# Kernel tuning notes

Measured on AMD Instinct MI355X. Metric: run time of the kernel, lower is better.

## Reference

```python
import jax, jax.numpy as jnp
import numpy as np

B, N, VF, EF, DV, DE, LN = 64, 64, 32, 16, 128, 128, 4
EPS_INNER = 128.0  # BatchNorm1d(MAX_N, internal_d_vert): 2nd positional arg is eps (faithful to source bug)
EPS_BN = 1e-5


def gev_layer(v_in, e_in, evW, evb, eW, eb, vW, vb, relu=True):
    act = jax.nn.relu if relu else (lambda x: x)
    ev = v_in @ evW + evb                                   # [B,N,De]
    # outer_v_sum: ev.unsqueeze(1) + ev.unsqueeze(2) -> [B,N,N,De]
    e_out = act(e_in @ eW + eb + ev[:, None, :, :] + ev[:, :, None, :])
    per_v_e = e_out.sum(axis=1)                             # sum-aggregate over dim 1
    v_out = act(jnp.concatenate([per_v_e, v_in], axis=-1) @ vW + vb)
    return v_out, e_out


def bn_flat(v, g, b):
    # BatchNorm1d(N*VF) on [B, N*VF] in training mode (biased var)
    x = v.reshape(-1, N * VF)
    mu = x.mean(axis=0)
    var = x.var(axis=0)
    x = (x - mu) * jax.lax.rsqrt(var + EPS_BN) * g + b
    return x.reshape(-1, N, VF)


def bn_inner(v, g, b):
    # BatchNorm1d(MAX_N, eps=128) on [B, N, D]: channels are the N axis, stats over (B, D)
    mu = v.mean(axis=(0, 2), keepdims=True)
    var = v.var(axis=(0, 2), keepdims=True)
    return (v - mu) * jax.lax.rsqrt(var + EPS_INNER) * g[None, :, None] + b[None, :, None]


def setup_inputs() -> dict:
    key = jax.random.key(0)
    ks = jax.random.split(key, 24)
    s = 0.01  # force_lin_init with init_noise=0.01, biases zero
    nrm = lambda k, shp: jax.random.normal(k, shp, dtype=jnp.float32) * s
    inp = {
        "v": jax.random.normal(ks[0], (B, N, VF), dtype=jnp.float32),
        "e": jax.random.normal(ks[1], (B, N, N, EF), dtype=jnp.float32),
        "bn_in_g": jnp.ones((N * VF,), jnp.float32),
        "bn_in_b": jnp.zeros((N * VF,), jnp.float32),
        "g1_evW": nrm(ks[2], (VF, DE)), "g1_evb": jnp.zeros((DE,), jnp.float32),
        "g1_eW": nrm(ks[3], (EF, DE)), "g1_eb": jnp.zeros((DE,), jnp.float32),
        "g1_vW": nrm(ks[4], (VF + DE, DV)), "g1_vb": jnp.zeros((DV,), jnp.float32),
        "inn_evW": nrm(ks[5], (LN, DV, DE)), "inn_evb": jnp.zeros((LN, DE), jnp.float32),
        "inn_eW": nrm(ks[6], (LN, DE, DE)), "inn_eb": jnp.zeros((LN, DE), jnp.float32),
        "inn_vW": nrm(ks[7], (LN, DV + DE, DV)), "inn_vb": jnp.zeros((LN, DV), jnp.float32),
        "bn_g": jnp.ones((LN, N), jnp.float32),
        "bn_b": jnp.zeros((LN, N), jnp.float32),
        "g3_evW": nrm(ks[8], (DV, 1)), "g3_evb": jnp.zeros((1,), jnp.float32),
        "g3_eW": nrm(ks[9], (DE, 1)), "g3_eb": jnp.zeros((1,), jnp.float32),
        "g3_vW": nrm(ks[10], (DV + 1, 1)), "g3_vb": jnp.zeros((1,), jnp.float32),
    }
    return inp


def reference(v, e, bn_in_g, bn_in_b, g1_evW, g1_evb, g1_eW, g1_eb, g1_vW, g1_vb,
              inn_evW, inn_evb, inn_eW, inn_eb, inn_vW, inn_vb, bn_g, bn_b,
              g3_evW, g3_evb, g3_eW, g3_eb, g3_vW, g3_vb):
    v = bn_flat(v, bn_in_g, bn_in_b)
    v, e = gev_layer(v, e, g1_evW, g1_evb, g1_eW, g1_eb, g1_vW, g1_vb)
    for i in range(LN):
        v_next, e_next = gev_layer(v, e, inn_evW[i], inn_evb[i], inn_eW[i], inn_eb[i], inn_vW[i], inn_vb[i])
        v = v_next + v  # resnet
        e = e_next + e
        v = bn_inner(v, bn_g[i], bn_b[i])
    v, e = gev_layer(v, e, g3_evW, g3_evb, g3_eW, g3_eb, g3_vW, g3_vb, relu=False)
    return v, e
```

## Files before the change

### kernel.cpp

```cpp
#include <hip/hip_runtime.h>
#include <hip/hip_bf16.h>


typedef __bf16 bf16_t;
typedef __bf16 bf16x8 __attribute__((ext_vector_type(8)));
typedef __bf16 bf16x4 __attribute__((ext_vector_type(4)));
typedef float f32x4 __attribute__((ext_vector_type(4)));

__device__ __forceinline__ void bar_lgkm() {
  asm volatile("s_waitcnt lgkmcnt(0)\n\ts_barrier" ::: "memory");
}

__global__ __launch_bounds__(256) void k_prep(const float* __restrict__ vin,
    const float* __restrict__ g, const float* __restrict__ bt,
    const float* __restrict__ eW, float* __restrict__ v0,
    bf16_t* __restrict__ Wt, float* __restrict__ pve3, float* __restrict__ stats) {
  const int blk = blockIdx.x, tid = threadIdx.x;
  if (blk < 8) {
    int ch = blk * 256 + tid;
    float s = 0.f, s2 = 0.f;
    for (int b = 0; b < 64; ++b) { float x = vin[b * 2048 + ch]; s += x; s2 += x * x; }
    float mu = s * (1.f / 64.f);
    float var = s2 * (1.f / 64.f) - mu * mu;
    float sc = rsqrtf(var + 1e-5f) * g[ch];
    float bb = bt[ch];
    for (int b = 0; b < 64; ++b) {
      float x = vin[b * 2048 + ch];
      v0[b * 2048 + ch] = (x - mu) * sc + bb;
    }
  } else if (blk < 264) {
    int idx = (blk - 8) * 256 + tid;
    int l = idx >> 14, r = idx & 16383, n = r >> 7, k = r & 127;
    Wt[idx] = (bf16_t)eW[(l << 14) + (k << 7) + n];
  } else {
    for (int i = tid; i < 4096; i += 256) pve3[i] = 0.f;
    for (int i = tid; i < 512; i += 256) stats[i] = 0.f;
  }
}

template <int K>
__global__ __launch_bounds__(128) void k_ev(const float* __restrict__ v_in,
    const float* __restrict__ W, const float* __restrict__ bias,
    float* __restrict__ out) {
  __shared__ float rows[8][K];
  const int r0 = blockIdx.x * 8;
  const int c = threadIdx.x;
  for (int idx = c; idx < 8 * K; idx += 128) {
    int rr = idx / K, kk = idx % K;
    rows[rr][kk] = v_in[(r0 + rr) * K + kk];
  }
  __syncthreads();
  float acc[8];
  const float bv = bias[c];
#pragma unroll
  for (int r = 0; r < 8; ++r) acc[r] = bv;
  for (int k4 = 0; k4 < K; k4 += 4) {
    float w0 = W[(k4 + 0) * 128 + c], w1 = W[(k4 + 1) * 128 + c];
    float w2 = W[(k4 + 2) * 128 + c], w3 = W[(k4 + 3) * 128 + c];
#pragma unroll
    for (int r = 0; r < 8; ++r) {
      float4 x = *(const float4*)&rows[r][k4];
      acc[r] += x.x * w0 + x.y * w1 + x.z * w2 + x.w * w3;
    }
  }
#pragma unroll
  for (int r = 0; r < 8; ++r) out[(r0 + r) * 128 + c] = acc[r];
}

__global__ __launch_bounds__(128) void k_evbn(float* __restrict__ v,
    const float* __restrict__ stats, const float* __restrict__ g,
    const float* __restrict__ bt, const float* __restrict__ W,
    const float* __restrict__ bias, float* __restrict__ out) {
  __shared__ float rows[8][128];
  const int r0 = blockIdx.x * 8;
  const int c = threadIdx.x;
#pragma unroll
  for (int rr = 0; rr < 8; ++rr) {
    int n = (r0 + rr) & 63;
    float mu = stats[n] * (1.f / 8192.f);
    float var = stats[64 + n] * (1.f / 8192.f) - mu * mu;
    float sc = rsqrtf(var + 128.f) * g[n];
    float x = (v[(r0 + rr) * 128 + c] - mu) * sc + bt[n];
    rows[rr][c] = x;
    v[(r0 + rr) * 128 + c] = x;
  }
  __syncthreads();
  float acc[8];
  const float bv = bias[c];
#pragma unroll
  for (int r = 0; r < 8; ++r) acc[r] = bv;
  for (int k4 = 0; k4 < 128; k4 += 4) {
    float w0 = W[(k4 + 0) * 128 + c], w1 = W[(k4 + 1) * 128 + c];
    float w2 = W[(k4 + 2) * 128 + c], w3 = W[(k4 + 3) * 128 + c];
#pragma unroll
    for (int r = 0; r < 8; ++r) {
      float4 x = *(const float4*)&rows[r][k4];
      acc[r] += x.x * w0 + x.y * w1 + x.z * w2 + x.w * w3;
    }
  }
#pragma unroll
  for (int r = 0; r < 8; ++r) out[(r0 + r) * 128 + c] = acc[r];
}

__global__ __launch_bounds__(256) void k_edge_g1(const float* __restrict__ e0,
    const float* __restrict__ eW, const float* __restrict__ eb,
    const float* __restrict__ ev, bf16_t* __restrict__ e_ws,
    float* __restrict__ pve) {
  __shared__ bf16_t A0s[2][64][40];
  __shared__ bf16_t Os[2][64][136];
  const int b = blockIdx.x >> 5, j0 = (blockIdx.x & 31) * 2;
  const int tid = threadIdx.x;
  const int lane = tid & 63, w = tid >> 6;
  const int quad = lane >> 4, l16 = lane & 15;
#pragma unroll
  for (int t = 0; t < 2; ++t) {
    int idx = tid + t * 256;
    int row = idx >> 3, off = (idx & 7) * 4;
    int jc = off >> 4, k = off & 15;
    f32x4 x = *(const f32x4*)&e0[((b * 64 + row) * 64 + j0) * 16 + off];
    bf16x4 y;
#pragma unroll
    for (int r = 0; r < 4; ++r) y[r] = (bf16_t)x[r];
    *(bf16x4*)&A0s[jc][row][k] = y;
    bf16x4 z = {(bf16_t)0.f, (bf16_t)0.f, (bf16_t)0.f, (bf16_t)0.f};
    *(bf16x4*)&A0s[jc][row][16 + k] = z;
  }
  const int c0[2] = {w * 32 + quad * 4, w * 32 + 16 + quad * 4};
  bf16x8 wf[2];
#pragma unroll
  for (int nt = 0; nt < 2; ++nt) {
    const int c = w * 32 + nt * 16 + l16;
#pragma unroll
    for (int jj = 0; jj < 8; ++jj)
      wf[nt][jj] = (quad < 2) ? (bf16_t)eW[(quad * 8 + jj) * 128 + c] : (bf16_t)0.f;
  }
  f32x4 acc[2][4][2];
  {
    f32x4 ebv[2], evj[2][2], evi[4][2];
#pragma unroll
    for (int nt = 0; nt < 2; ++nt) {
      ebv[nt] = *(const f32x4*)&eb[c0[nt]];
#pragma unroll
      for (int jc = 0; jc < 2; ++jc)
        evj[jc][nt] = *(const f32x4*)&ev[(b * 64 + j0 + jc) * 128 + c0[nt]];
#pragma unroll
      for (int mt = 0; mt < 4; ++mt)
        evi[mt][nt] = *(const f32x4*)&ev[(b * 64 + mt * 16 + l16) * 128 + c0[nt]];
    }
#pragma unroll
    for (int jc = 0; jc < 2; ++jc)
#pragma unroll
      for (int mt = 0; mt < 4; ++mt)
#pragma unroll
        for (int nt = 0; nt < 2; ++nt)
          acc[jc][mt][nt] = ebv[nt] + evj[jc][nt] + evi[mt][nt];
  }
  __syncthreads();
#pragma unroll
  for (int jc = 0; jc < 2; ++jc) {
#pragma unroll
    for (int mt = 0; mt < 4; ++mt) {
      bf16x8 ef = *(const bf16x8*)&A0s[jc][mt * 16 + l16][quad * 8];
#pragma unroll
      for (int nt = 0; nt < 2; ++nt)
        acc[jc][mt][nt] = __builtin_amdgcn_mfma_f32_16x16x32_bf16(wf[nt], ef, acc[jc][mt][nt], 0, 0, 0);
    }
  }
#pragma unroll
  for (int jc = 0; jc < 2; ++jc) {
#pragma unroll
    for (int nt = 0; nt < 2; ++nt) {
      f32x4 ps = {0.f, 0.f, 0.f, 0.f};
#pragma unroll
      for (int mt = 0; mt < 4; ++mt) {
        const int i = mt * 16 + l16;
        bf16x4 outv;
#pragma unroll
        for (int r = 0; r < 4; ++r) {
          float vv = fmaxf(acc[jc][mt][nt][r], 0.f);
          ps[r] += vv;
          outv[r] = (bf16_t)vv;
        }
        *(bf16x4*)&Os[jc][i][c0[nt]] = outv;
      }
#pragma unroll
      for (int m = 1; m <= 8; m <<= 1) {
#pragma unroll
        for (int r = 0; r < 4; ++r) ps[r] += __shfl_xor(ps[r], m);
      }
      if (l16 == 0) *(f32x4*)&pve[(b * 64 + j0 + jc) * 128 + c0[nt]] = ps;
    }
  }
  __syncthreads();
#pragma unroll
  for (int t = 0; t < 8; ++t) {
    int idx = tid + t * 256;
    int row = idx >> 5, off = (idx & 31) * 8;
    int jc = off >> 7, c = off & 127;
    *(int4*)&e_ws[((b * 64 + row) * 64 + j0) * 128 + off] = *(const int4*)&Os[jc][row][c];
  }
}

__global__ __launch_bounds__(128) void k_v_g1(const float* __restrict__ pve,
    const float* __restrict__ v0, const float* __restrict__ vW,
    const float* __restrict__ vb, float* __restrict__ v) {
  __shared__ float in[8][160];
  const int r0 = blockIdx.x * 8;
  const int c = threadIdx.x;
#pragma unroll
  for (int t = 0; t < 8; ++t) {
    int idx = c + t * 128;
    int rr = idx >> 7, k = idx & 127;
    in[rr][k] = pve[(r0 + rr) * 128 + k];
  }
#pragma unroll
  for (int t = 0; t < 2; ++t) {
    int idx = c + t * 128;
    int rr = idx >> 5, k = idx & 31;
    in[rr][128 + k] = v0[(r0 + rr) * 32 + k];
  }
  __syncthreads();
  float acc[8];
  const float bv = vb[c];
#pragma unroll
  for (int r = 0; r < 8; ++r) acc[r] = bv;
  for (int k4 = 0; k4 < 160; k4 += 4) {
    float w0 = vW[(k4 + 0) * 128 + c], w1 = vW[(k4 + 1) * 128 + c];
    float w2 = vW[(k4 + 2) * 128 + c], w3 = vW[(k4 + 3) * 128 + c];
#pragma unroll
    for (int r = 0; r < 8; ++r) {
      float4 x = *(const float4*)&in[r][k4];
      acc[r] += x.x * w0 + x.y * w1 + x.z * w2 + x.w * w3;
    }
  }
#pragma unroll
  for (int r = 0; r < 8; ++r) v[(r0 + r) * 128 + c] = fmaxf(acc[r], 0.f);
}

__global__ __launch_bounds__(256) void k_edge_inner(bf16_t* __restrict__ e_ws,
    const bf16_t* __restrict__ Wt, const float* __restrict__ eb,
    const float* __restrict__ ev, float* __restrict__ pve) {
  __shared__ bf16_t As[2][64][136];
  const int tid = threadIdx.x;
  const int lane = tid & 63, w = tid >> 6;
  const int quad = lane >> 4, l16 = lane & 15;
  const int b = blockIdx.x >> 4;
  const int jb = (blockIdx.x & 15) * 4;
  const int c0[2] = {w * 32 + quad * 4, w * 32 + 16 + quad * 4};
  bf16x8 wf[2][4];
#pragma unroll
  for (int nt = 0; nt < 2; ++nt)
#pragma unroll
    for (int ks = 0; ks < 4; ++ks)
      wf[nt][ks] = *(const bf16x8*)&Wt[(w * 32 + nt * 16 + l16) * 128 + ks * 32 + quad * 8];
  f32x4 ebv[2], evi[4][2];
#pragma unroll
  for (int nt = 0; nt < 2; ++nt) {
    ebv[nt] = *(const f32x4*)&eb[c0[nt]];
#pragma unroll
    for (int mt = 0; mt < 4; ++mt)
      evi[mt][nt] = *(const f32x4*)&ev[(b * 64 + mt * 16 + l16) * 128 + c0[nt]];
  }
  int4 stg[4];
  f32x4 evj[2];
#pragma unroll
  for (int u = 0; u < 4; ++u) {
    int idx = tid + u * 256;
    stg[u] = *(const int4*)&e_ws[((b * 64 + (idx >> 4)) * 64 + jb) * 128 + (idx & 15) * 8];
  }
#pragma unroll
  for (int nt = 0; nt < 2; ++nt)
    evj[nt] = *(const f32x4*)&ev[(b * 64 + jb) * 128 + c0[nt]];
#pragma unroll
  for (int u = 0; u < 4; ++u) {
    int idx = tid + u * 256;
    *(int4*)&As[0][idx >> 4][(idx & 15) * 8] = stg[u];
  }
  bar_lgkm();
#pragma unroll
  for (int t = 0; t < 4; ++t) {
    const int X = t & 1, j = jb + t;
    int4 stg2[4];
    f32x4 evj2[2];
    if (t < 3) {
#pragma unroll
      for (int u = 0; u < 4; ++u) {
        int idx = tid + u * 256;
        stg2[u] = *(const int4*)&e_ws[((b * 64 + (idx >> 4)) * 64 + (j + 1)) * 128 + (idx & 15) * 8];
      }
#pragma unroll
      for (int nt = 0; nt < 2; ++nt)
        evj2[nt] = *(const f32x4*)&ev[(b * 64 + j + 1) * 128 + c0[nt]];
    }
    f32x4 acc[4][2];
#pragma unroll
    for (int mt = 0; mt < 4; ++mt)
#pragma unroll
      for (int nt = 0; nt < 2; ++nt)
        acc[mt][nt] = ebv[nt] + evj[nt] + evi[mt][nt];
#pragma unroll
    for (int ks = 0; ks < 4; ++ks) {
      bf16x8 ef[4];
#pragma unroll
      for (int mt = 0; mt < 4; ++mt)
        ef[mt] = *(const bf16x8*)&As[X][mt * 16 + l16][ks * 32 + quad * 8];
#pragma unroll
      for (int mt = 0; mt < 4; ++mt)
#pragma unroll
        for (int nt = 0; nt < 2; ++nt)
          acc[mt][nt] = __builtin_amdgcn_mfma_f32_16x16x32_bf16(wf[nt][ks], ef[mt], acc[mt][nt], 0, 0, 0);
    }
    bar_lgkm();
#pragma unroll
    for (int nt = 0; nt < 2; ++nt) {
      f32x4 ps = {0.f, 0.f, 0.f, 0.f};
#pragma unroll
      for (int mt = 0; mt < 4; ++mt) {
        const int i = mt * 16 + l16;
        bf16x4 eo = *(const bf16x4*)&As[X][i][c0[nt]];
        bf16x4 outv;
#pragma unroll
        for (int r = 0; r < 4; ++r) {
          float vv = fmaxf(acc[mt][nt][r], 0.f);
          ps[r] += vv;
          outv[r] = (bf16_t)(vv + (float)eo[r]);
        }
        *(bf16x4*)&As[X][i][c0[nt]] = outv;
      }
#pragma unroll
      for (int m = 1; m <= 8; m <<= 1) {
#pragma unroll
        for (int r = 0; r < 4; ++r) ps[r] += __shfl_xor(ps[r], m);
      }
      if (l16 == 0) *(f32x4*)&pve[(b * 64 + j) * 128 + c0[nt]] = ps;
    }
    bar_lgkm();
#pragma unroll
    for (int u = 0; u < 4; ++u) {
      int idx = tid + u * 256;
      *(int4*)&e_ws[((b * 64 + (idx >> 4)) * 64 + j) * 128 + (idx & 15) * 8] =
          *(const int4*)&As[X][idx >> 4][(idx & 15) * 8];
    }
    if (t < 3) {
#pragma unroll
      for (int u = 0; u < 4; ++u) {
        int idx = tid + u * 256;
        *(int4*)&As[1 - X][idx >> 4][(idx & 15) * 8] = stg2[u];
      }
      evj[0] = evj2[0];
      evj[1] = evj2[1];
    }
    bar_lgkm();
  }
}

__global__ __launch_bounds__(128) void k_v_inner(const float* __restrict__ pve,
    float* __restrict__ v, const float* __restrict__ vW,
    const float* __restrict__ vb, float* __restrict__ stats) {
  __shared__ float in[8][256];
  __shared__ float outs[8][132];
  const int r0 = blockIdx.x * 8;
  const int c = threadIdx.x;
#pragma unroll
  for (int t = 0; t < 8; ++t) {
    int idx = c + t * 128;
    int rr = idx >> 7, k = idx & 127;
    in[rr][k] = pve[(r0 + rr) * 128 + k];
    in[rr][128 + k] = v[(r0 + rr) * 128 + k];
  }
  __syncthreads();
  float acc[8];
  const float bv = vb[c];
#pragma unroll
  for (int r = 0; r < 8; ++r) acc[r] = bv;
  for (int k4 = 0; k4 < 256; k4 += 4) {
    float w0 = vW[(k4 + 0) * 128 + c], w1 = vW[(k4 + 1) * 128 + c];
    float w2 = vW[(k4 + 2) * 128 + c], w3 = vW[(k4 + 3) * 128 + c];
#pragma unroll
    for (int r = 0; r < 8; ++r) {
      float4 x = *(const float4*)&in[r][k4];
      acc[r] += x.x * w0 + x.y * w1 + x.z * w2 + x.w * w3;
    }
  }
#pragma unroll
  for (int r = 0; r < 8; ++r) {
    float val = fmaxf(acc[r], 0.f) + in[r][128 + c];
    outs[r][c] = val;
    v[(r0 + r) * 128 + c] = val;
  }
  __syncthreads();
  if (c < 8) {
    float s = 0.f, s2 = 0.f;
    for (int k = 0; k < 128; ++k) { float x = outs[c][k]; s += x; s2 += x * x; }
    int n = (r0 + c) & 63;
    atomicAdd(&stats[n], s);
    atomicAdd(&stats[64 + n], s2);
  }
}

__global__ __launch_bounds__(256) void k_edge_g3(const bf16_t* __restrict__ e_ws,
    const float* __restrict__ vv, const float* __restrict__ stats3,
    const float* __restrict__ g, const float* __restrict__ bt,
    const float* __restrict__ evW3, const float* __restrict__ evb3,
    const float* __restrict__ eW3, const float* __restrict__ eb3,
    float* __restrict__ out_e, float* __restrict__ pve3) {
  __shared__ float vbn[64][132];
  __shared__ float scs[64], shs[64];
  __shared__ float W3e[128], W3ee[128];
  __shared__ float ev3s[64];
  const int b = blockIdx.x >> 6, i = blockIdx.x & 63;
  const int tid = threadIdx.x;
  if (tid < 64) {
    float mu = stats3[tid] * (1.f / 8192.f);
    float var = stats3[64 + tid] * (1.f / 8192.f) - mu * mu;
    float sc = rsqrtf(var + 128.f) * g[tid];
    scs[tid] = sc;
    shs[tid] = bt[tid] - mu * sc;
  }
  if (tid < 128) W3ee[tid] = eW3[tid];
  else W3e[tid - 128] = evW3[tid - 128];
  __syncthreads();
#pragma unroll
  for (int t = 0; t < 8; ++t) {
    int idx = t * 1024 + tid * 4;
    int row = idx >> 7, c = idx & 127;
    f32x4 x = *(const f32x4*)&vv[(b * 64 + row) * 128 + c];
    f32x4 y = x * scs[row] + shs[row];
    *(f32x4*)&vbn[row][c] = y;
  }
  __syncthreads();
  {
    int r = tid >> 2, q = tid & 3;
    float a = 0.f;
#pragma unroll
    for (int u = 0; u < 32; ++u) a += vbn[r][q * 32 + u] * W3e[q * 32 + u];
    a += __shfl_xor(a, 1);
    a += __shfl_xor(a, 2);
    if (q == 0) ev3s[r] = a + evb3[0];
  }
  __syncthreads();
  {
    const int j = tid >> 2, cs = (tid & 3) * 32;
    const bf16_t* ep = &e_ws[(size_t)((b * 64 + i) * 64 + j) * 128 + cs];
    float acc = 0.f;
#pragma unroll
    for (int t = 0; t < 4; ++t) {
      bf16x8 x = *(const bf16x8*)&ep[t * 8];
#pragma unroll
      for (int u = 0; u < 8; ++u) acc += (float)x[u] * W3ee[cs + t * 8 + u];
    }
    acc += __shfl_xor(acc, 1);
    acc += __shfl_xor(acc, 2);
    if ((tid & 3) == 0) {
      float s = acc + eb3[0] + ev3s[i] + ev3s[j];
      out_e[(b * 64 + i) * 64 + j] = s;
      atomicAdd(&pve3[b * 64 + j], s);
    }
  }
}

__global__ __launch_bounds__(256) void k_v_g3(const float* __restrict__ vv,
    const float* __restrict__ stats3, const float* __restrict__ g,
    const float* __restrict__ bt, const float* __restrict__ pve3,
    const float* __restrict__ vW, const float* __restrict__ vb,
    float* __restrict__ out_v) {
  int r = blockIdx.x * 4 + (threadIdx.x >> 6);
  int lane = threadIdx.x & 63;
  int n = r & 63;
  float mu = stats3[n] * (1.f / 8192.f);
  float var = stats3[64 + n] * (1.f / 8192.f) - mu * mu;
  float sc = rsqrtf(var + 128.f) * g[n];
  float sh = bt[n] - mu * sc;
  float x1 = vv[r * 128 + lane] * sc + sh;
  float x2 = vv[r * 128 + 64 + lane] * sc + sh;
  float acc = x1 * vW[1 + lane] + x2 * vW[65 + lane];
#pragma unroll
  for (int m = 1; m < 64; m <<= 1) acc += __shfl_xor(acc, m);
  if (lane == 0) out_v[r] = acc + pve3[r] * vW[0] + vb[0];
}

extern "C" void kernel_launch(void* const* d_in, const int* in_sizes, int n_in,
                              void* d_out, int out_size, void* d_ws, size_t ws_size,
                              hipStream_t stream) {
  const float* in_v    = (const float*)d_in[0];
  const float* in_e    = (const float*)d_in[1];
  const float* bn_in_g = (const float*)d_in[2];
  const float* bn_in_b = (const float*)d_in[3];
  const float* g1_evW  = (const float*)d_in[4];
  const float* g1_evb  = (const float*)d_in[5];
  const float* g1_eW   = (const float*)d_in[6];
  const float* g1_eb   = (const float*)d_in[7];
  const float* g1_vW   = (const float*)d_in[8];
  const float* g1_vb   = (const float*)d_in[9];
  const float* inn_evW = (const float*)d_in[10];
  const float* inn_evb = (const float*)d_in[11];
  const float* inn_eW  = (const float*)d_in[12];
  const float* inn_eb  = (const float*)d_in[13];
  const float* inn_vW  = (const float*)d_in[14];
  const float* inn_vb  = (const float*)d_in[15];
  const float* bn_g    = (const float*)d_in[16];
  const float* bn_b    = (const float*)d_in[17];
  const float* g3_evW  = (const float*)d_in[18];
  const float* g3_evb  = (const float*)d_in[19];
  const float* g3_eW   = (const float*)d_in[20];
  const float* g3_eb   = (const float*)d_in[21];
  const float* g3_vW   = (const float*)d_in[22];
  const float* g3_vb   = (const float*)d_in[23];

  char* ws = (char*)d_ws;
  bf16_t* e_ws = (bf16_t*)(ws);
  float* v     = (float*)(ws + 67108864);
  float* ev    = (float*)(ws + 69206016);
  float* pve   = (float*)(ws + 71303168);
  float* v0    = (float*)(ws + 73400320);
  bf16_t* Wt   = (bf16_t*)(ws + 73924608);
  float* pve3  = (float*)(ws + 74072064);
  float* stats = (float*)(ws + 74088448);

  float* out_v = (float*)d_out;
  float* out_e = (float*)d_out + 4096;

  k_prep<<<265, 256, 0, stream>>>(in_v, bn_in_g, bn_in_b, inn_eW, v0, Wt, pve3, stats);

  k_ev<32><<<512, 128, 0, stream>>>(v0, g1_evW, g1_evb, ev);
  k_edge_g1<<<2048, 256, 0, stream>>>(in_e, g1_eW, g1_eb, ev, e_ws, pve);
  k_v_g1<<<512, 128, 0, stream>>>(pve, v0, g1_vW, g1_vb, v);

  for (int l = 0; l < 4; ++l) {
    if (l == 0)
      k_ev<128><<<512, 128, 0, stream>>>(v, inn_evW, inn_evb, ev);
    else
      k_evbn<<<512, 128, 0, stream>>>(v, stats + (l - 1) * 128, bn_g + (l - 1) * 64,
                                      bn_b + (l - 1) * 64, inn_evW + l * 16384,
                                      inn_evb + l * 128, ev);
    k_edge_inner<<<1024, 256, 0, stream>>>(e_ws, Wt + l * 16384, inn_eb + l * 128, ev, pve);
    k_v_inner<<<512, 128, 0, stream>>>(pve, v, inn_vW + l * 32768, inn_vb + l * 128,
                                       stats + l * 128);
  }

  k_edge_g3<<<4096, 256, 0, stream>>>(e_ws, v, stats + 384, bn_g + 192, bn_b + 192,
                                      g3_evW, g3_evb, g3_eW, g3_eb, out_e, pve3);
  k_v_g3<<<1024, 256, 0, stream>>>(v, stats + 384, bn_g + 192, bn_b + 192, pve3,
                                   g3_vW, g3_vb, out_v);
}
```

Measured before the change: 457.1 us.

## Fuse final edge projection into last inner layer and merge g3 kernels

The last inner edge kernel now computes the g3 edge dot product (e·eW3) directly from shared memory and writes a small per-edge scalar, so the final bf16 edge tensor is never written back or reread. The two g3 kernels become one per-batch kernel that builds out_e and the per-vertex sums without atomics, which also drops the pve3 zeroing. The first inner ev projection is fused into the g1 vertex kernel. The edge kernel also handles two j columns per stage with a larger LDS buffer, which may lower occupancy.

```diff
diff --git a/kernel.cpp b/kernel.cpp
--- a/kernel.cpp
+++ b/kernel.cpp
@@ -14,7 +14,7 @@
 __global__ __launch_bounds__(256) void k_prep(const float* __restrict__ vin,
     const float* __restrict__ g, const float* __restrict__ bt,
     const float* __restrict__ eW, float* __restrict__ v0,
-    bf16_t* __restrict__ Wt, float* __restrict__ pve3, float* __restrict__ stats) {
+    bf16_t* __restrict__ Wt, float* __restrict__ stats) {
   const int blk = blockIdx.x, tid = threadIdx.x;
   if (blk < 8) {
     int ch = blk * 256 + tid;
@@ -33,7 +33,6 @@
     int l = idx >> 14, r = idx & 16383, n = r >> 7, k = r & 127;
     Wt[idx] = (bf16_t)eW[(l << 14) + (k << 7) + n];
   } else {
-    for (int i = tid; i < 4096; i += 256) pve3[i] = 0.f;
     for (int i = tid; i < 512; i += 256) stats[i] = 0.f;
   }
 }
@@ -201,10 +200,12 @@
   }
 }
 
-__global__ __launch_bounds__(128) void k_v_g1(const float* __restrict__ pve,
+__global__ __launch_bounds__(128) void k_vg1_ev(const float* __restrict__ pve,
     const float* __restrict__ v0, const float* __restrict__ vW,
-    const float* __restrict__ vb, float* __restrict__ v) {
+    const float* __restrict__ vb, const float* __restrict__ evW,
+    const float* __restrict__ evb, float* __restrict__ v, float* __restrict__ ev) {
   __shared__ float in[8][160];
+  __shared__ float vr[8][128];
   const int r0 = blockIdx.x * 8;
   const int c = threadIdx.x;
 #pragma unroll
@@ -234,18 +235,41 @@
     }
   }
 #pragma unroll
-  for (int r = 0; r < 8; ++r) v[(r0 + r) * 128 + c] = fmaxf(acc[r], 0.f);
-}
-
+  for (int r = 0; r < 8; ++r) {
+    float val = fmaxf(acc[r], 0.f);
+    vr[r][c] = val;
+    v[(r0 + r) * 128 + c] = val;
+  }
+  __syncthreads();
+  float acc2[8];
+  const float bv2 = evb[c];
+#pragma unroll
+  for (int r = 0; r < 8; ++r) acc2[r] = bv2;
+  for (int k4 = 0; k4 < 128; k4 += 4) {
+    float w0 = evW[(k4 + 0) * 128 + c], w1 = evW[(k4 + 1) * 128 + c];
+    float w2 = evW[(k4 + 2) * 128 + c], w3 = evW[(k4 + 3) * 128 + c];
+#pragma unroll
+    for (int r = 0; r < 8; ++r) {
+      float4 x = *(const float4*)&vr[r][k4];
+      acc2[r] += x.x * w0 + x.y * w1 + x.z * w2 + x.w * w3;
+    }
+  }
+#pragma unroll
+  for (int r = 0; r < 8; ++r) ev[(r0 + r) * 128 + c] = acc2[r];
+}
+
+template <bool LAST>
 __global__ __launch_bounds__(256) void k_edge_inner(bf16_t* __restrict__ e_ws,
     const bf16_t* __restrict__ Wt, const float* __restrict__ eb,
-    const float* __restrict__ ev, float* __restrict__ pve) {
-  __shared__ bf16_t As[2][64][136];
+    const float* __restrict__ ev, float* __restrict__ pve,
+    const float* __restrict__ eW3, float* __restrict__ edt) {
+  __shared__ bf16_t As[2][2][64][136];
+  __shared__ float W3s[128];
   const int tid = threadIdx.x;
   const int lane = tid & 63, w = tid >> 6;
   const int quad = lane >> 4, l16 = lane & 15;
   const int b = blockIdx.x >> 4;
-  const int jb = (blockIdx.x & 15) * 4;
+  const int jg = (blockIdx.x & 15) * 4;
   const int c0[2] = {w * 32 + quad * 4, w * 32 + 16 + quad * 4};
   bf16x8 wf[2][4];
 #pragma unroll
@@ -261,96 +285,131 @@
     for (int mt = 0; mt < 4; ++mt)
       evi[mt][nt] = *(const f32x4*)&ev[(b * 64 + mt * 16 + l16) * 128 + c0[nt]];
   }
-  int4 stg[4];
-  f32x4 evj[2];
-#pragma unroll
-  for (int u = 0; u < 4; ++u) {
+  if (LAST) {
+    if (tid < 128) W3s[tid] = eW3[tid];
+  }
+  int4 stg[8];
+#pragma unroll
+  for (int u = 0; u < 8; ++u) {
     int idx = tid + u * 256;
-    stg[u] = *(const int4*)&e_ws[((b * 64 + (idx >> 4)) * 64 + jb) * 128 + (idx & 15) * 8];
-  }
-#pragma unroll
-  for (int nt = 0; nt < 2; ++nt)
-    evj[nt] = *(const f32x4*)&ev[(b * 64 + jb) * 128 + c0[nt]];
-#pragma unroll
-  for (int u = 0; u < 4; ++u) {
+    stg[u] = *(const int4*)&e_ws[((b * 64 + (idx >> 5)) * 64 + jg) * 128 + (idx & 31) * 8];
+  }
+  f32x4 evj[2][2];
+#pragma unroll
+  for (int jc = 0; jc < 2; ++jc)
+#pragma unroll
+    for (int nt = 0; nt < 2; ++nt)
+      evj[jc][nt] = *(const f32x4*)&ev[(b * 64 + jg + jc) * 128 + c0[nt]];
+#pragma unroll
+  for (int u = 0; u < 8; ++u) {
     int idx = tid + u * 256;
-    *(int4*)&As[0][idx >> 4][(idx & 15) * 8] = stg[u];
+    int off = (idx & 31) * 8;
+    *(int4*)&As[0][off >> 7][idx >> 5][off & 127] = stg[u];
   }
   bar_lgkm();
 #pragma unroll
-  for (int t = 0; t < 4; ++t) {
-    const int X = t & 1, j = jb + t;
-    int4 stg2[4];
-    f32x4 evj2[2];
-    if (t < 3) {
-#pragma unroll
-      for (int u = 0; u < 4; ++u) {
+  for (int p = 0; p < 2; ++p) {
+    const int j0 = jg + p * 2;
+    int4 stg2[8];
+    f32x4 evj2[2][2];
+    if (p == 0) {
+#pragma unroll
+      for (int u = 0; u < 8; ++u) {
         int idx = tid + u * 256;
-        stg2[u] = *(const int4*)&e_ws[((b * 64 + (idx >> 4)) * 64 + (j + 1)) * 128 + (idx & 15) * 8];
-      }
-#pragma unroll
-      for (int nt = 0; nt < 2; ++nt)
-        evj2[nt] = *(const f32x4*)&ev[(b * 64 + j + 1) * 128 + c0[nt]];
-    }
-    f32x4 acc[4][2];
-#pragma unroll
-    for (int mt = 0; mt < 4; ++mt)
-#pragma unroll
-      for (int nt = 0; nt < 2; ++nt)
-        acc[mt][nt] = ebv[nt] + evj[nt] + evi[mt][nt];
+        stg2[u] = *(const int4*)&e_ws[((b * 64 + (idx >> 5)) * 64 + jg + 2) * 128 + (idx & 31) * 8];
+      }
+#pragma unroll
+      for (int jc = 0; jc < 2; ++jc)
+#pragma unroll
+        for (int nt = 0; nt < 2; ++nt)
+          evj2[jc][nt] = *(const f32x4*)&ev[(b * 64 + jg + 2 + jc) * 128 + c0[nt]];
+    }
+    f32x4 acc[2][4][2];
+#pragma unroll
+    for (int jc = 0; jc < 2; ++jc)
+#pragma unroll
+      for (int mt = 0; mt < 4; ++mt)
+#pragma unroll
+        for (int nt = 0; nt < 2; ++nt)
+          acc[jc][mt][nt] = ebv[nt] + evj[jc][nt] + evi[mt][nt];
 #pragma unroll
     for (int ks = 0; ks < 4; ++ks) {
-      bf16x8 ef[4];
-#pragma unroll
-      for (int mt = 0; mt < 4; ++mt)
-        ef[mt] = *(const bf16x8*)&As[X][mt * 16 + l16][ks * 32 + quad * 8];
-#pragma unroll
-      for (int mt = 0; mt < 4; ++mt)
-#pragma unroll
-        for (int nt = 0; nt < 2; ++nt)
-          acc[mt][nt] = __builtin_amdgcn_mfma_f32_16x16x32_bf16(wf[nt][ks], ef[mt], acc[mt][nt], 0, 0, 0);
+      bf16x8 ef[2][4];
+#pragma unroll
+      for (int jc = 0; jc < 2; ++jc)
+#pragma unroll
+        for (int mt = 0; mt < 4; ++mt)
+          ef[jc][mt] = *(const bf16x8*)&As[p][jc][mt * 16 + l16][ks * 32 + quad * 8];
+#pragma unroll
+      for (int jc = 0; jc < 2; ++jc)
+#pragma unroll
+        for (int mt = 0; mt < 4; ++mt)
+#pragma unroll
+          for (int nt = 0; nt < 2; ++nt)
+            acc[jc][mt][nt] = __builtin_amdgcn_mfma_f32_16x16x32_bf16(wf[nt][ks], ef[jc][mt], acc[jc][mt][nt], 0, 0, 0);
     }
     bar_lgkm();
 #pragma unroll
-    for (int nt = 0; nt < 2; ++nt) {
-      f32x4 ps = {0.f, 0.f, 0.f, 0.f};
-#pragma unroll
-      for (int mt = 0; mt < 4; ++mt) {
-        const int i = mt * 16 + l16;
-        bf16x4 eo = *(const bf16x4*)&As[X][i][c0[nt]];
-        bf16x4 outv;
-#pragma unroll
-        for (int r = 0; r < 4; ++r) {
-          float vv = fmaxf(acc[mt][nt][r], 0.f);
-          ps[r] += vv;
-          outv[r] = (bf16_t)(vv + (float)eo[r]);
+    for (int jc = 0; jc < 2; ++jc) {
+#pragma unroll
+      for (int nt = 0; nt < 2; ++nt) {
+        f32x4 ps = {0.f, 0.f, 0.f, 0.f};
+#pragma unroll
+        for (int mt = 0; mt < 4; ++mt) {
+          const int i = mt * 16 + l16;
+          bf16x4 eo = *(const bf16x4*)&As[p][jc][i][c0[nt]];
+          bf16x4 outv;
+#pragma unroll
+          for (int r = 0; r < 4; ++r) {
+            float vv = fmaxf(acc[jc][mt][nt][r], 0.f);
+            ps[r] += vv;
+            outv[r] = (bf16_t)(vv + (float)eo[r]);
+          }
+          *(bf16x4*)&As[p][jc][i][c0[nt]] = outv;
         }
-        *(bf16x4*)&As[X][i][c0[nt]] = outv;
-      }
-#pragma unroll
-      for (int m = 1; m <= 8; m <<= 1) {
-#pragma unroll
-        for (int r = 0; r < 4; ++r) ps[r] += __shfl_xor(ps[r], m);
-      }
-      if (l16 == 0) *(f32x4*)&pve[(b * 64 + j) * 128 + c0[nt]] = ps;
+#pragma unroll
+        for (int m = 1; m <= 8; m <<= 1) {
+#pragma unroll
+          for (int r = 0; r < 4; ++r) ps[r] += __shfl_xor(ps[r], m);
+        }
+        if (l16 == 0) *(f32x4*)&pve[(b * 64 + j0 + jc) * 128 + c0[nt]] = ps;
+      }
     }
     bar_lgkm();
-#pragma unroll
-    for (int u = 0; u < 4; ++u) {
-      int idx = tid + u * 256;
-      *(int4*)&e_ws[((b * 64 + (idx >> 4)) * 64 + j) * 128 + (idx & 15) * 8] =
-          *(const int4*)&As[X][idx >> 4][(idx & 15) * 8];
-    }
-    if (t < 3) {
-#pragma unroll
-      for (int u = 0; u < 4; ++u) {
+    if (!LAST) {
+#pragma unroll
+      for (int u = 0; u < 8; ++u) {
         int idx = tid + u * 256;
-        *(int4*)&As[1 - X][idx >> 4][(idx & 15) * 8] = stg2[u];
-      }
-      evj[0] = evj2[0];
-      evj[1] = evj2[1];
-    }
-    bar_lgkm();
+        int off = (idx & 31) * 8;
+        *(int4*)&e_ws[((b * 64 + (idx >> 5)) * 64 + j0) * 128 + off] =
+            *(const int4*)&As[p][off >> 7][idx >> 5][off & 127];
+      }
+    } else {
+      const int i = tid >> 2, q = tid & 3;
+#pragma unroll
+      for (int jc = 0; jc < 2; ++jc) {
+        float d = 0.f;
+#pragma unroll
+        for (int u = 0; u < 32; ++u) d += (float)As[p][jc][i][q * 32 + u] * W3s[q * 32 + u];
+        d += __shfl_xor(d, 1);
+        d += __shfl_xor(d, 2);
+        if (q == 0) edt[(b * 64 + j0 + jc) * 64 + i] = d;
+      }
+    }
+    if (p == 0) {
+#pragma unroll
+      for (int u = 0; u < 8; ++u) {
+        int idx = tid + u * 256;
+        int off = (idx & 31) * 8;
+        *(int4*)&As[1][off >> 7][idx >> 5][off & 127] = stg2[u];
+      }
+#pragma unroll
+      for (int jc = 0; jc < 2; ++jc) {
+        evj[jc][0] = evj2[jc][0];
+        evj[jc][1] = evj2[jc][1];
+      }
+      bar_lgkm();
+    }
   }
 }
 
@@ -398,18 +457,21 @@
   }
 }
 
-__global__ __launch_bounds__(256) void k_edge_g3(const bf16_t* __restrict__ e_ws,
-    const float* __restrict__ vv, const float* __restrict__ stats3,
-    const float* __restrict__ g, const float* __restrict__ bt,
-    const float* __restrict__ evW3, const float* __restrict__ evb3,
-    const float* __restrict__ eW3, const float* __restrict__ eb3,
-    float* __restrict__ out_e, float* __restrict__ pve3) {
+__global__ __launch_bounds__(256) void k_g3(const float* __restrict__ vv,
+    const float* __restrict__ stats3, const float* __restrict__ g,
+    const float* __restrict__ bt, const float* __restrict__ evW3,
+    const float* __restrict__ evb3, const float* __restrict__ eb3,
+    const float* __restrict__ edt, const float* __restrict__ vW3,
+    const float* __restrict__ vb3, float* __restrict__ out_v,
+    float* __restrict__ out_e) {
   __shared__ float vbn[64][132];
+  __shared__ float edts[64][68];
   __shared__ float scs[64], shs[64];
-  __shared__ float W3e[128], W3ee[128];
+  __shared__ float W3e[128];
+  __shared__ float vWs[132];
   __shared__ float ev3s[64];
-  const int b = blockIdx.x >> 6, i = blockIdx.x & 63;
-  const int tid = threadIdx.x;
+  __shared__ float pj[4][64];
+  const int b = blockIdx.x, tid = threadIdx.x;
   if (tid < 64) {
     float mu = stats3[tid] * (1.f / 8192.f);
     float var = stats3[64 + tid] * (1.f / 8192.f) - mu * mu;
@@ -417,66 +479,60 @@
     scs[tid] = sc;
     shs[tid] = bt[tid] - mu * sc;
   }
-  if (tid < 128) W3ee[tid] = eW3[tid];
-  else W3e[tid - 128] = evW3[tid - 128];
+  if (tid < 128) W3e[tid] = evW3[tid];
+  if (tid < 129) vWs[tid] = vW3[tid];
   __syncthreads();
 #pragma unroll
   for (int t = 0; t < 8; ++t) {
     int idx = t * 1024 + tid * 4;
-    int row = idx >> 7, c = idx & 127;
-    f32x4 x = *(const f32x4*)&vv[(b * 64 + row) * 128 + c];
-    f32x4 y = x * scs[row] + shs[row];
-    *(f32x4*)&vbn[row][c] = y;
+    int row = idx >> 7, cc = idx & 127;
+    f32x4 x = *(const f32x4*)&vv[(b * 64 + row) * 128 + cc];
+    *(f32x4*)&vbn[row][cc] = x * scs[row] + shs[row];
+  }
+#pragma unroll
+  for (int t = 0; t < 4; ++t) {
+    int idx = t * 1024 + tid * 4;
+    int j = idx >> 6, i = idx & 63;
+    *(f32x4*)&edts[j][i] = *(const f32x4*)&edt[(b * 64 + j) * 64 + i];
   }
   __syncthreads();
   {
-    int r = tid >> 2, q = tid & 3;
-    float a = 0.f;
-#pragma unroll
-    for (int u = 0; u < 32; ++u) a += vbn[r][q * 32 + u] * W3e[q * 32 + u];
-    a += __shfl_xor(a, 1);
-    a += __shfl_xor(a, 2);
-    if (q == 0) ev3s[r] = a + evb3[0];
+    int i = tid >> 2, q = tid & 3;
+    float d = 0.f;
+#pragma unroll
+    for (int u = 0; u < 32; ++u) d += vbn[i][q * 32 + u] * W3e[q * 32 + u];
+    d += __shfl_xor(d, 1);
+    d += __shfl_xor(d, 2);
+    if (q == 0) ev3s[i] = d + evb3[0];
   }
   __syncthreads();
   {
-    const int j = tid >> 2, cs = (tid & 3) * 32;
-    const bf16_t* ep = &e_ws[(size_t)((b * 64 + i) * 64 + j) * 128 + cs];
-    float acc = 0.f;
-#pragma unroll
-    for (int t = 0; t < 4; ++t) {
-      bf16x8 x = *(const bf16x8*)&ep[t * 8];
-#pragma unroll
-      for (int u = 0; u < 8; ++u) acc += (float)x[u] * W3ee[cs + t * 8 + u];
-    }
-    acc += __shfl_xor(acc, 1);
-    acc += __shfl_xor(acc, 2);
-    if ((tid & 3) == 0) {
-      float s = acc + eb3[0] + ev3s[i] + ev3s[j];
-      out_e[(b * 64 + i) * 64 + j] = s;
-      atomicAdd(&pve3[b * 64 + j], s);
-    }
-  }
-}
-
-__global__ __launch_bounds__(256) void k_v_g3(const float* __restrict__ vv,
-    const float* __restrict__ stats3, const float* __restrict__ g,
-    const float* __restrict__ bt, const float* __restrict__ pve3,
-    const float* __restrict__ vW, const float* __restrict__ vb,
-    float* __restrict__ out_v) {
-  int r = blockIdx.x * 4 + (threadIdx.x >> 6);
-  int lane = threadIdx.x & 63;
-  int n = r & 63;
-  float mu = stats3[n] * (1.f / 8192.f);
-  float var = stats3[64 + n] * (1.f / 8192.f) - mu * mu;
-  float sc = rsqrtf(var + 128.f) * g[n];
-  float sh = bt[n] - mu * sc;
-  float x1 = vv[r * 128 + lane] * sc + sh;
-  float x2 = vv[r * 128 + 64 + lane] * sc + sh;
-  float acc = x1 * vW[1 + lane] + x2 * vW[65 + lane];
-#pragma unroll
-  for (int m = 1; m < 64; m <<= 1) acc += __shfl_xor(acc, m);
-  if (lane == 0) out_v[r] = acc + pve3[r] * vW[0] + vb[0];
+    int q = tid >> 6, j = tid & 63;
+    float s = 0.f;
+    const float e3 = eb3[0];
+    const float evj = ev3s[j];
+#pragma unroll
+    for (int r = 0; r < 16; ++r) {
+      int i = q * 16 + r;
+      float val = edts[j][i] + e3 + ev3s[i] + evj;
+      out_e[(b * 64 + i) * 64 + j] = val;
+      s += val;
+    }
+    pj[q][j] = s;
+  }
+  __syncthreads();
+  {
+    int n = tid >> 2, q = tid & 3;
+    float d = 0.f;
+#pragma unroll
+    for (int u = 0; u < 32; ++u) d += vbn[n][q * 32 + u] * vWs[1 + q * 32 + u];
+    d += __shfl_xor(d, 1);
+    d += __shfl_xor(d, 2);
+    if (q == 0) {
+      float p3 = pj[0][n] + pj[1][n] + pj[2][n] + pj[3][n];
+      out_v[b * 64 + n] = d + p3 * vWs[0] + vb3[0];
+    }
+  }
 }
 
 extern "C" void kernel_launch(void* const* d_in, const int* in_sizes, int n_in,
@@ -514,32 +570,34 @@
   float* pve   = (float*)(ws + 71303168);
   float* v0    = (float*)(ws + 73400320);
   bf16_t* Wt   = (bf16_t*)(ws + 73924608);
-  float* pve3  = (float*)(ws + 74072064);
-  float* stats = (float*)(ws + 74088448);
+  float* edt   = (float*)(ws + 74055680);
+  float* stats = (float*)(ws + 75104256);
 
   float* out_v = (float*)d_out;
   float* out_e = (float*)d_out + 4096;
 
-  k_prep<<<265, 256, 0, stream>>>(in_v, bn_in_g, bn_in_b, inn_eW, v0, Wt, pve3, stats);
+  k_prep<<<265, 256, 0, stream>>>(in_v, bn_in_g, bn_in_b, inn_eW, v0, Wt, stats);
 
   k_ev<32><<<512, 128, 0, stream>>>(v0, g1_evW, g1_evb, ev);
   k_edge_g1<<<2048, 256, 0, stream>>>(in_e, g1_eW, g1_eb, ev, e_ws, pve);
-  k_v_g1<<<512, 128, 0, stream>>>(pve, v0, g1_vW, g1_vb, v);
+  k_vg1_ev<<<512, 128, 0, stream>>>(pve, v0, g1_vW, g1_vb, inn_evW, inn_evb, v, ev);
 
   for (int l = 0; l < 4; ++l) {
-    if (l == 0)
-      k_ev<128><<<512, 128, 0, stream>>>(v, inn_evW, inn_evb, ev);
-    else
+    if (l > 0)
       k_evbn<<<512, 128, 0, stream>>>(v, stats + (l - 1) * 128, bn_g + (l - 1) * 64,
                                       bn_b + (l - 1) * 64, inn_evW + l * 16384,
                                       inn_evb + l * 128, ev);
-    k_edge_inner<<<1024, 256, 0, stream>>>(e_ws, Wt + l * 16384, inn_eb + l * 128, ev, pve);
+    if (l < 3)
+      k_edge_inner<false><<<1024, 256, 0, stream>>>(e_ws, Wt + l * 16384,
+          inn_eb + l * 128, ev, pve, g3_eW, edt);
+    else
+      k_edge_inner<true><<<1024, 256, 0, stream>>>(e_ws, Wt + l * 16384,
+          inn_eb + l * 128, ev, pve, g3_eW, edt);
     k_v_inner<<<512, 128, 0, stream>>>(pve, v, inn_vW + l * 32768, inn_vb + l * 128,
                                        stats + l * 128);
   }
 
-  k_edge_g3<<<4096, 256, 0, stream>>>(e_ws, v, stats + 384, bn_g + 192, bn_b + 192,
-                                      g3_evW, g3_evb, g3_eW, g3_eb, out_e, pve3);
-  k_v_g3<<<1024, 256, 0, stream>>>(v, stats + 384, bn_g + 192, bn_b + 192, pve3,
-                                   g3_vW, g3_vb, out_v);
-}
+  k_g3<<<64, 256, 0, stream>>>(v, stats + 384, bn_g + 192, bn_b + 192,
+                               g3_evW, g3_evb, g3_eb, edt, g3_vW, g3_vb,
+                               out_v, out_e);
+}
```

Result: no change. 455.1 us (-0.4%).
